# Performance work log

Measured on AMD Instinct MI355X. Metric: run time of the kernel, lower is better.

The kernel has to match this reference:

```python
import jax, jax.numpy as jnp
import numpy as np

B, S, HID = 2, 2048, 2048
H, KV, D, E = 16, 4, 128, 32
NB = 9  # num_behavior + 1
EPS = 1e-6
SCALING = (E + D) ** -0.5


def rmsnorm(x, w, eps=EPS):
    # normalize over last dim in fp32, like Qwen3MoeRMSNorm
    xf = x.astype(jnp.float32)
    var = jnp.mean(xf * xf, axis=-1, keepdims=True)
    return (xf * jax.lax.rsqrt(var + eps)).astype(x.dtype) * w


def setup_inputs() -> dict:
    key = jax.random.key(0)
    ks = jax.random.split(key, 12)
    s = lambda n: 1.0 / np.sqrt(n)
    return {
        "hidden_states": jax.random.normal(ks[0], (B, S, HID), jnp.float32),
        "behavior_index": jax.random.randint(ks[1], (B, S), 0, NB),
        "q_proj_w": jax.random.normal(ks[2], (H * D, HID), jnp.float32) * s(HID),
        "k_proj_w": jax.random.normal(ks[3], (KV * D, HID), jnp.float32) * s(HID),
        "v_proj_w": jax.random.normal(ks[4], (KV * D, HID), jnp.float32) * s(HID),
        "o_proj_w": jax.random.normal(ks[5], (HID, H * D), jnp.float32) * s(H * D),
        "q_norm_w": jnp.ones((D,), jnp.float32),
        "k_norm_w": jnp.ones((D,), jnp.float32),
        "qbe_table": jax.random.normal(ks[6], (NB, H * E), jnp.float32),
        "kbe_table": jax.random.normal(ks[7], (NB, KV * E), jnp.float32),
        "qbn_w": jnp.ones((E,), jnp.float32),
        "kbn_w": jnp.ones((E,), jnp.float32),
    }


def reference(hidden_states, behavior_index, q_proj_w, k_proj_w, v_proj_w,
              o_proj_w, q_norm_w, k_norm_w, qbe_table, kbe_table, qbn_w, kbn_w):
    b, s, _ = hidden_states.shape
    # QKV projections + per-head RMSNorm on q/k
    q = rmsnorm((hidden_states @ q_proj_w.T).reshape(b, s, H, D), q_norm_w)
    k = rmsnorm((hidden_states @ k_proj_w.T).reshape(b, s, KV, D), k_norm_w)
    v = (hidden_states @ v_proj_w.T).reshape(b, s, KV, D)
    q = q.transpose(0, 2, 1, 3)  # [b,H,s,D]
    k = k.transpose(0, 2, 1, 3)  # [b,KV,s,D]
    v = v.transpose(0, 2, 1, 3)  # [b,KV,s,D]
    # behavior embeddings: lookup -> per-head RMSNorm -> concat onto head_dim
    qbe = rmsnorm(qbe_table[behavior_index].reshape(b, s, H, E), qbn_w).transpose(0, 2, 1, 3)
    kbe = rmsnorm(kbe_table[behavior_index].reshape(b, s, KV, E), kbn_w).transpose(0, 2, 1, 3)
    q = jnp.concatenate([q, qbe], axis=-1)  # [b,H,s,D+E]
    k = jnp.concatenate([k, kbe], axis=-1)  # [b,KV,s,D+E]
    # GQA: repeat kv heads
    g = H // KV
    k = jnp.repeat(k, g, axis=1)
    v = jnp.repeat(v, g, axis=1)
    # eager attention, causal, softmax in fp32
    scores = jnp.einsum('bhqd,bhkd->bhqk', q, k) * SCALING
    causal = jnp.tril(jnp.ones((s, s), bool))
    scores = jnp.where(causal, scores, jnp.finfo(scores.dtype).min)
    attn = jax.nn.softmax(scores.astype(jnp.float32), axis=-1).astype(q.dtype)
    out = jnp.einsum('bhqk,bhkd->bhqd', attn, v)  # [b,H,s,D]
    out = out.transpose(0, 2, 1, 3).reshape(b, s, H * D)
    return out @ o_proj_w.T
```

## Files before the change

### kernel.cpp

```cpp
#include <hip/hip_runtime.h>

typedef unsigned short u16;
typedef unsigned int u32;
typedef __bf16 bf16x8 __attribute__((ext_vector_type(8)));
typedef __bf16 b16x4 __attribute__((ext_vector_type(4)));
typedef short s16x4 __attribute__((ext_vector_type(4)));
typedef float f32x4 __attribute__((ext_vector_type(4)));

#define SCALE 0.07905694150420949f
#define LOG2E 1.4426950408889634f

__device__ __forceinline__ float bf2f(u16 h) { return __uint_as_float(((u32)h) << 16); }
__device__ __forceinline__ u16 f2bf(float f) {
  u32 u = __float_as_uint(f);
  u += 0x7fffu + ((u >> 16) & 1u);
  return (u16)(u >> 16);
}
__device__ __forceinline__ u16 f2bf_fast(float f) {
  return (u16)((__float_as_uint(f) + 0x8000u) >> 16);
}
__device__ __forceinline__ bf16x8 ldfrag(const u16* p) {
  int4 t = *reinterpret_cast<const int4*>(p);
  return __builtin_bit_cast(bf16x8, t);
}

__device__ __forceinline__ f32x4 mfma16x16(s16x4 a, s16x4 b, f32x4 c) {
#if __has_builtin(__builtin_amdgcn_mfma_f32_16x16x16bf16_1k)
  return __builtin_amdgcn_mfma_f32_16x16x16bf16_1k(a, b, c, 0, 0, 0);
#elif __has_builtin(__builtin_amdgcn_mfma_f32_16x16x16_bf16)
  return __builtin_amdgcn_mfma_f32_16x16x16_bf16(__builtin_bit_cast(b16x4, a),
                                                 __builtin_bit_cast(b16x4, b), c, 0, 0, 0);
#else
  asm volatile("s_nop 2\n\tv_mfma_f32_16x16x16_bf16 %0, %1, %2, %0"
               : "+v"(c) : "v"(a), "v"(b));
  return c;
#endif
}

__device__ __forceinline__ void gld16(const u16* g, u16* l) {
  __builtin_amdgcn_global_load_lds((const __attribute__((address_space(1))) u32*)(const void*)g,
                                   (__attribute__((address_space(3))) u32*)(void*)l, 16, 0, 0);
}

__global__ void conv_f32_bf16(const float* __restrict__ in, u16* __restrict__ out, int n) {
  int n4 = n >> 2;
  for (int i = blockIdx.x * blockDim.x + threadIdx.x; i < n4; i += gridDim.x * blockDim.x) {
    float4 v = reinterpret_cast<const float4*>(in)[i];
    ushort4 o = {f2bf(v.x), f2bf(v.y), f2bf(v.z), f2bf(v.w)};
    reinterpret_cast<ushort4*>(out)[i] = o;
  }
}

template <int OUT_BF16>
__global__ __launch_bounds__(256, 2) void gemm_bt(const u16* __restrict__ A,
                                                  const u16* __restrict__ Bw,
                                                  void* __restrict__ Cv,
                                                  int M, int N, int K) {
  __shared__ __align__(16) u16 As[2][8192];
  __shared__ __align__(16) u16 Bs[2][8192];
  const int tid = threadIdx.x;
  const int nbn = N >> 7;
  const int cpx = gridDim.x >> 3;
  const int swz = (blockIdx.x & 7) * cpx + (blockIdx.x >> 3);
  const int bm = swz / nbn, bn = swz % nbn;
  const int row0 = bm << 7, col0 = bn << 7;
  const int lane = tid & 63, w = tid >> 6;
  const int lg = lane >> 4, lr = lane & 15;
  const int wr = w >> 1, wc = w & 1;
  const int nt = K >> 6;

  auto stage = [&](int slot, int t) {
    const size_t k0 = (size_t)t << 6;
#pragma unroll
    for (int it = 0; it < 4; ++it) {
      int G = it * 256 + tid;
      int r = G >> 3, p = G & 7;
      int gs = p ^ (r & 7);
      gld16(&A[(size_t)(row0 + r) * K + k0 + gs * 8], &As[slot][(size_t)G * 8]);
      gld16(&Bw[(size_t)(col0 + r) * K + k0 + gs * 8], &Bs[slot][(size_t)G * 8]);
    }
  };

  f32x4 acc[4][4] = {};
  stage(0, 0);
  if (nt > 1) stage(1, 1);

  for (int t = 0; t < nt; ++t) {
    const int slot = t & 1;
    if (t + 1 < nt) {
      asm volatile("s_waitcnt vmcnt(8)" ::: "memory");
    } else {
      asm volatile("s_waitcnt vmcnt(0)" ::: "memory");
    }
    __builtin_amdgcn_s_barrier();
    __builtin_amdgcn_sched_barrier(0);
#pragma unroll
    for (int kk = 0; kk < 2; ++kk) {
      bf16x8 af[4], bv[4];
#pragma unroll
      for (int m = 0; m < 4; ++m) {
        int r = wr * 64 + m * 16 + lr;
        int g = (kk * 4 + lg) ^ (lr & 7);
        af[m] = ldfrag(&As[slot][r * 64 + g * 8]);
      }
#pragma unroll
      for (int n = 0; n < 4; ++n) {
        int r = wc * 64 + n * 16 + lr;
        int g = (kk * 4 + lg) ^ (lr & 7);
        bv[n] = ldfrag(&Bs[slot][r * 64 + g * 8]);
      }
#pragma unroll
      for (int m = 0; m < 4; ++m)
#pragma unroll
        for (int n = 0; n < 4; ++n)
          acc[m][n] = __builtin_amdgcn_mfma_f32_16x16x32_bf16(af[m], bv[n], acc[m][n], 0, 0, 0);
    }
    __builtin_amdgcn_sched_barrier(0);
    __builtin_amdgcn_s_barrier();
    if (t + 2 < nt) stage(slot, t + 2);
  }

#pragma unroll
  for (int m = 0; m < 4; ++m)
#pragma unroll
    for (int n = 0; n < 4; ++n)
#pragma unroll
      for (int r = 0; r < 4; ++r) {
        int row = row0 + wr * 64 + m * 16 + lg * 4 + r;
        int col = col0 + wc * 64 + n * 16 + lr;
        float v = acc[m][n][r];
        if (OUT_BF16)
          ((u16*)Cv)[(size_t)row * N + col] = f2bf(v);
        else
          ((float*)Cv)[(size_t)row * N + col] = v;
      }
}

__global__ __launch_bounds__(256) void postproc(
    const u16* __restrict__ qkv, const int* __restrict__ bidx,
    const float* __restrict__ qnw, const float* __restrict__ knw,
    const float* __restrict__ qbe_t, const float* __restrict__ kbe_t,
    const float* __restrict__ qbn, const float* __restrict__ kbn,
    u16* __restrict__ qcat, u16* __restrict__ kcat, u16* __restrict__ vt) {
  const int tok = blockIdx.x;
  const int b = tok >> 11, s = tok & 2047;
  const int w = threadIdx.x >> 6, lane = threadIdx.x & 63;
  const int idx = bidx[tok];
  const u16* base = qkv + (size_t)tok * 3072;
  const float QS = SCALE * LOG2E;

  for (int h = w; h < 16; h += 4) {
    float x0 = bf2f(base[h * 128 + 2 * lane]);
    float x1 = bf2f(base[h * 128 + 2 * lane + 1]);
    float ss = x0 * x0 + x1 * x1;
#pragma unroll
    for (int o = 32; o; o >>= 1) ss += __shfl_xor(ss, o);
    float rn = rsqrtf(ss * (1.f / 128.f) + 1e-6f) * QS;
    size_t ob = ((size_t)(b * 16 + h) * 2048 + s) * 160;
    qcat[ob + 2 * lane] = f2bf(x0 * rn * qnw[2 * lane]);
    qcat[ob + 2 * lane + 1] = f2bf(x1 * rn * qnw[2 * lane + 1]);
    if (lane < 32) {
      float e = qbe_t[idx * 512 + h * 32 + lane];
      float s2 = e * e;
#pragma unroll
      for (int o = 16; o; o >>= 1) s2 += __shfl_xor(s2, o);
      qcat[ob + 128 + lane] = f2bf(e * rsqrtf(s2 * (1.f / 32.f) + 1e-6f) * qbn[lane] * QS);
    }
  }
  {
    const int kv = w;
    float x0 = bf2f(base[2048 + kv * 128 + 2 * lane]);
    float x1 = bf2f(base[2048 + kv * 128 + 2 * lane + 1]);
    float ss = x0 * x0 + x1 * x1;
#pragma unroll
    for (int o = 32; o; o >>= 1) ss += __shfl_xor(ss, o);
    float rn = rsqrtf(ss * (1.f / 128.f) + 1e-6f);
    size_t ob = ((size_t)(b * 4 + kv) * 2048 + s) * 160;
    kcat[ob + 2 * lane] = f2bf(x0 * rn * knw[2 * lane]);
    kcat[ob + 2 * lane + 1] = f2bf(x1 * rn * knw[2 * lane + 1]);
    if (lane < 32) {
      float e = kbe_t[idx * 128 + kv * 32 + lane];
      float s2 = e * e;
#pragma unroll
      for (int o = 16; o; o >>= 1) s2 += __shfl_xor(s2, o);
      kcat[ob + 128 + lane] = f2bf(e * rsqrtf(s2 * (1.f / 32.f) + 1e-6f) * kbn[lane]);
    }
    size_t vb = (size_t)(b * 4 + kv) * 128 * 2048;
    vt[vb + (size_t)lane * 2048 + s] = base[2560 + kv * 128 + lane];
    vt[vb + (size_t)(lane + 64) * 2048 + s] = base[2560 + kv * 128 + 64 + lane];
  }
}

__global__ __launch_bounds__(256, 2) void attn(const u16* __restrict__ qcat,
                                               const u16* __restrict__ kcat,
                                               const u16* __restrict__ vt,
                                               u16* __restrict__ aout) {
  __shared__ __align__(16) u16 Kls[2][10240];
  __shared__ __align__(16) u16 Vls[8192];
  const int tid = threadIdx.x;
  const int blk = blockIdx.x;
  const int kvh = blk & 3;
  const int b = (blk >> 2) & 1;
  const int hq = (blk >> 3) & 3;
  const int g = blk >> 5;
  const int h = kvh * 4 + hq;
  const int w = tid >> 6;
  const int lane = tid & 63;
  const int lg = lane >> 4, lr = lane & 15;
  const int qb_a = g * 4 + w;
  const int qb_b = 127 - qb_a;
  const int qpa = qb_a * 16 + lr;
  const int qpb = qb_b * 16 + lr;
  const int nt = 32 - g;

  const u16* qpA = qcat + ((size_t)(b * 16 + h) * 2048 + qb_a * 16) * 160;
  const u16* qpB = qcat + ((size_t)(b * 16 + h) * 2048 + qb_b * 16) * 160;
  bf16x8 qfa[5], qfb[5];
#pragma unroll
  for (int c = 0; c < 5; ++c) {
    qfa[c] = ldfrag(qpA + lr * 160 + c * 32 + lg * 8);
    qfb[c] = ldfrag(qpB + lr * 160 + c * 32 + lg * 8);
  }

  const u16* kbp = kcat + (size_t)(b * 4 + kvh) * 2048 * 160;
  const u16* vbp = vt + (size_t)(b * 4 + kvh) * 128 * 2048;

  auto stageK = [&](int buf, int kt) {
    const u16* ksrc = kbp + (size_t)kt * (64 * 160);
#pragma unroll
    for (int it = 0; it < 5; ++it) {
      int G = it * 256 + tid;
      int r = G / 20, p = G - r * 20;
      int gs = p ^ ((r >> 1) & 3);
      gld16(ksrc + r * 160 + gs * 8, &Kls[buf][G * 8]);
    }
  };
  auto stageV = [&](int kt) {
    const u16* vsrc = vbp + kt * 64;
#pragma unroll
    for (int it = 0; it < 4; ++it) {
      int G = it * 256 + tid;
      int r = G >> 3, p = G & 7;
      int gs = p ^ (r & 7);
      gld16(vsrc + (size_t)r * 2048 + gs * 8, &Vls[G * 8]);
    }
  };

  float ma = -INFINITY, la = 0.f, mb = -INFINITY, lb = 0.f;
  f32x4 acc_a[8] = {}, acc_b[8] = {};

  stageK(0, 0);
  stageV(0);
  __syncthreads();

  for (int kt = 0; kt < nt; ++kt) {
    const int buf = kt & 1;
    const bool aact = (kt <= g);
    if (kt + 1 < nt) stageK(buf ^ 1, kt + 1);

    f32x4 sa[4] = {}, sb[4] = {};
#pragma unroll
    for (int c = 0; c < 5; ++c) {
      bf16x8 kf[4];
#pragma unroll
      for (int i = 0; i < 4; ++i) {
        int r = i * 16 + lr;
        int p = (c * 4 + lg) ^ ((r >> 1) & 3);
        kf[i] = ldfrag(&Kls[buf][(r * 20 + p) * 8]);
      }
#pragma unroll
      for (int i = 0; i < 4; ++i)
        sb[i] = __builtin_amdgcn_mfma_f32_16x16x32_bf16(kf[i], qfb[c], sb[i], 0, 0, 0);
      if (aact)
#pragma unroll
        for (int i = 0; i < 4; ++i)
          sa[i] = __builtin_amdgcn_mfma_f32_16x16x32_bf16(kf[i], qfa[c], sa[i], 0, 0, 0);
    }

    s16x4 pka[4], pkb[4];
    auto soft = [&](f32x4 (&st)[4], float& mm, float& ls, f32x4 (&ac)[8], s16x4 (&pk)[4],
                    bool masked, int qpos) {
      float vmax = -INFINITY;
#pragma unroll
      for (int i = 0; i < 4; ++i)
#pragma unroll
        for (int r = 0; r < 4; ++r) {
          float v = st[i][r];
          if (masked && (kt * 64 + i * 16 + 4 * lg + r > qpos)) v = -INFINITY;
          st[i][r] = v;
          vmax = fmaxf(vmax, v);
        }
      vmax = fmaxf(vmax, __shfl_xor(vmax, 16));
      vmax = fmaxf(vmax, __shfl_xor(vmax, 32));
      bool skip = __all(vmax <= mm + 8.f);
      float mn = skip ? mm : fmaxf(mm, vmax);
      float rs = 0.f;
#pragma unroll
      for (int i = 0; i < 4; ++i)
#pragma unroll
        for (int r = 0; r < 4; ++r) {
          float p = exp2f(st[i][r] - mn);
          st[i][r] = p;
          rs += p;
        }
      rs += __shfl_xor(rs, 16);
      rs += __shfl_xor(rs, 32);
      if (skip) {
        ls += rs;
      } else {
        float corr = exp2f(mm - mn);
        ls = ls * corr + rs;
        mm = mn;
        float c4[4];
#pragma unroll
        for (int r = 0; r < 4; ++r) c4[r] = __shfl(corr, 4 * lg + r);
#pragma unroll
        for (int dt = 0; dt < 8; ++dt)
#pragma unroll
          for (int r = 0; r < 4; ++r) ac[dt][r] *= c4[r];
      }
#pragma unroll
      for (int i = 0; i < 4; ++i) {
        pk[i][0] = (short)f2bf_fast(st[i][0]);
        pk[i][1] = (short)f2bf_fast(st[i][1]);
        pk[i][2] = (short)f2bf_fast(st[i][2]);
        pk[i][3] = (short)f2bf_fast(st[i][3]);
      }
    };
    soft(sb, mb, lb, acc_b, pkb, kt == nt - 1, qpb);
    if (aact) soft(sa, ma, la, acc_a, pka, kt == g, qpa);

    __syncthreads();

#pragma unroll
    for (int ks = 0; ks < 4; ++ks) {
      s16x4 vf[8];
#pragma unroll
      for (int dt = 0; dt < 8; ++dt) {
        int r = dt * 16 + lr;
        int p = (ks * 2 + (lg >> 1)) ^ (r & 7);
        vf[dt] = *reinterpret_cast<const s16x4*>(&Vls[(r * 8 + p) * 8 + (lg & 1) * 4]);
      }
#pragma unroll
      for (int dt = 0; dt < 8; ++dt) acc_b[dt] = mfma16x16(pkb[ks], vf[dt], acc_b[dt]);
      if (aact)
#pragma unroll
        for (int dt = 0; dt < 8; ++dt) acc_a[dt] = mfma16x16(pka[ks], vf[dt], acc_a[dt]);
    }

    __syncthreads();
    if (kt + 1 < nt) stageV(kt + 1);
  }

  float inva[4], invb[4];
#pragma unroll
  for (int r = 0; r < 4; ++r) {
    inva[r] = 1.f / __shfl(la, 4 * lg + r);
    invb[r] = 1.f / __shfl(lb, 4 * lg + r);
  }
#pragma unroll
  for (int dt = 0; dt < 8; ++dt)
#pragma unroll
    for (int r = 0; r < 4; ++r) {
      int rowa = qb_a * 16 + 4 * lg + r;
      int rowb = qb_b * 16 + 4 * lg + r;
      aout[((size_t)(b * 2048 + rowa) * 16 + h) * 128 + dt * 16 + lr] =
          f2bf(acc_a[dt][r] * inva[r]);
      aout[((size_t)(b * 2048 + rowb) * 16 + h) * 128 + dt * 16 + lr] =
          f2bf(acc_b[dt][r] * invb[r]);
    }
}

extern "C" void kernel_launch(void* const* d_in, const int* in_sizes, int n_in,
                              void* d_out, int out_size, void* d_ws, size_t ws_size,
                              hipStream_t stream) {
  const float* hs = (const float*)d_in[0];
  const int* bidx = (const int*)d_in[1];
  const float* qw = (const float*)d_in[2];
  const float* kw = (const float*)d_in[3];
  const float* vw = (const float*)d_in[4];
  const float* ow = (const float*)d_in[5];
  const float* qnw = (const float*)d_in[6];
  const float* knw = (const float*)d_in[7];
  const float* qbe_t = (const float*)d_in[8];
  const float* kbe_t = (const float*)d_in[9];
  const float* qbn = (const float*)d_in[10];
  const float* kbn = (const float*)d_in[11];

  u16* ws = (u16*)d_ws;
  u16* hs_bf = ws;
  u16* wqkv = hs_bf + 8388608;
  u16* ow_bf = wqkv + 6291456;
  u16* qkv = ow_bf + 4194304;
  u16* qcat = qkv + 12582912;
  u16* kcat = qcat + 10485760;
  u16* vt = kcat + 2621440;
  u16* attn_o = vt + 2097152;

  conv_f32_bf16<<<2048, 256, 0, stream>>>(hs, hs_bf, 8388608);
  conv_f32_bf16<<<1024, 256, 0, stream>>>(qw, wqkv, 4194304);
  conv_f32_bf16<<<512, 256, 0, stream>>>(kw, wqkv + 4194304, 1048576);
  conv_f32_bf16<<<512, 256, 0, stream>>>(vw, wqkv + 5242880, 1048576);
  conv_f32_bf16<<<1024, 256, 0, stream>>>(ow, ow_bf, 4194304);

  gemm_bt<1><<<dim3((4096 / 128) * (3072 / 128)), 256, 0, stream>>>(
      hs_bf, wqkv, (void*)qkv, 4096, 3072, 2048);

  postproc<<<4096, 256, 0, stream>>>(qkv, bidx, qnw, knw, qbe_t, kbe_t, qbn, kbn,
                                     qcat, kcat, vt);

  attn<<<512, 256, 0, stream>>>(qcat, kcat, vt, attn_o);

  gemm_bt<0><<<dim3((4096 / 128) * (2048 / 128)), 256, 0, stream>>>(
      attn_o, ow_bf, (void*)d_out, 4096, 2048, 2048);
}
```

Before: 229.3 us.

## Enlarge GEMM tiles to 256x256 with 512 threads and fuse conversion kernels

```diff
diff --git a/kernel.cpp b/kernel.cpp
--- a/kernel.cpp
+++ b/kernel.cpp
@@ -42,38 +42,55 @@
                                    (__attribute__((address_space(3))) u32*)(void*)l, 16, 0, 0);
 }
 
-__global__ void conv_f32_bf16(const float* __restrict__ in, u16* __restrict__ out, int n) {
-  int n4 = n >> 2;
-  for (int i = blockIdx.x * blockDim.x + threadIdx.x; i < n4; i += gridDim.x * blockDim.x) {
-    float4 v = reinterpret_cast<const float4*>(in)[i];
+__global__ void conv_all(const float* __restrict__ hs, const float* __restrict__ qw,
+                         const float* __restrict__ kw, const float* __restrict__ vw,
+                         const float* __restrict__ ow, u16* __restrict__ hs_bf,
+                         u16* __restrict__ wqkv, u16* __restrict__ ow_bf) {
+  const int total = 4718592;
+  for (int i = blockIdx.x * blockDim.x + threadIdx.x; i < total; i += gridDim.x * blockDim.x) {
+    const float* src;
+    u16* dst;
+    int j = i;
+    if (j < 2097152) {
+      src = hs; dst = hs_bf;
+    } else if (j < 3145728) {
+      j -= 2097152; src = qw; dst = wqkv;
+    } else if (j < 3407872) {
+      j -= 3145728; src = kw; dst = wqkv + 4194304;
+    } else if (j < 3670016) {
+      j -= 3407872; src = vw; dst = wqkv + 5242880;
+    } else {
+      j -= 3670016; src = ow; dst = ow_bf;
+    }
+    float4 v = reinterpret_cast<const float4*>(src)[j];
     ushort4 o = {f2bf(v.x), f2bf(v.y), f2bf(v.z), f2bf(v.w)};
-    reinterpret_cast<ushort4*>(out)[i] = o;
+    reinterpret_cast<ushort4*>(dst)[j] = o;
   }
 }
 
 template <int OUT_BF16>
-__global__ __launch_bounds__(256, 2) void gemm_bt(const u16* __restrict__ A,
+__global__ __launch_bounds__(512, 2) void gemm_bt(const u16* __restrict__ A,
                                                   const u16* __restrict__ Bw,
                                                   void* __restrict__ Cv,
                                                   int M, int N, int K) {
-  __shared__ __align__(16) u16 As[2][8192];
-  __shared__ __align__(16) u16 Bs[2][8192];
+  __shared__ __align__(16) u16 As[2][16384];
+  __shared__ __align__(16) u16 Bs[2][16384];
   const int tid = threadIdx.x;
-  const int nbn = N >> 7;
+  const int nbn = N >> 8;
   const int cpx = gridDim.x >> 3;
   const int swz = (blockIdx.x & 7) * cpx + (blockIdx.x >> 3);
   const int bm = swz / nbn, bn = swz % nbn;
-  const int row0 = bm << 7, col0 = bn << 7;
+  const int row0 = bm << 8, col0 = bn << 8;
   const int lane = tid & 63, w = tid >> 6;
   const int lg = lane >> 4, lr = lane & 15;
-  const int wr = w >> 1, wc = w & 1;
+  const int wr = w >> 2, wc = w & 3;
   const int nt = K >> 6;
 
   auto stage = [&](int slot, int t) {
     const size_t k0 = (size_t)t << 6;
 #pragma unroll
     for (int it = 0; it < 4; ++it) {
-      int G = it * 256 + tid;
+      int G = it * 512 + tid;
       int r = G >> 3, p = G & 7;
       int gs = p ^ (r & 7);
       gld16(&A[(size_t)(row0 + r) * K + k0 + gs * 8], &As[slot][(size_t)G * 8]);
@@ -81,7 +98,7 @@
     }
   };
 
-  f32x4 acc[4][4] = {};
+  f32x4 acc[8][4] = {};
   stage(0, 0);
   if (nt > 1) stage(1, 1);
 
@@ -96,10 +113,10 @@
     __builtin_amdgcn_sched_barrier(0);
 #pragma unroll
     for (int kk = 0; kk < 2; ++kk) {
-      bf16x8 af[4], bv[4];
-#pragma unroll
-      for (int m = 0; m < 4; ++m) {
-        int r = wr * 64 + m * 16 + lr;
+      bf16x8 af[8], bv[4];
+#pragma unroll
+      for (int m = 0; m < 8; ++m) {
+        int r = wr * 128 + m * 16 + lr;
         int g = (kk * 4 + lg) ^ (lr & 7);
         af[m] = ldfrag(&As[slot][r * 64 + g * 8]);
       }
@@ -110,7 +127,7 @@
         bv[n] = ldfrag(&Bs[slot][r * 64 + g * 8]);
       }
 #pragma unroll
-      for (int m = 0; m < 4; ++m)
+      for (int m = 0; m < 8; ++m)
 #pragma unroll
         for (int n = 0; n < 4; ++n)
           acc[m][n] = __builtin_amdgcn_mfma_f32_16x16x32_bf16(af[m], bv[n], acc[m][n], 0, 0, 0);
@@ -121,12 +138,12 @@
   }
 
 #pragma unroll
-  for (int m = 0; m < 4; ++m)
+  for (int m = 0; m < 8; ++m)
 #pragma unroll
     for (int n = 0; n < 4; ++n)
 #pragma unroll
       for (int r = 0; r < 4; ++r) {
-        int row = row0 + wr * 64 + m * 16 + lg * 4 + r;
+        int row = row0 + wr * 128 + m * 16 + lg * 4 + r;
         int col = col0 + wc * 64 + n * 16 + lr;
         float v = acc[m][n][r];
         if (OUT_BF16)
@@ -397,13 +414,9 @@
   u16* vt = kcat + 2621440;
   u16* attn_o = vt + 2097152;
 
-  conv_f32_bf16<<<2048, 256, 0, stream>>>(hs, hs_bf, 8388608);
-  conv_f32_bf16<<<1024, 256, 0, stream>>>(qw, wqkv, 4194304);
-  conv_f32_bf16<<<512, 256, 0, stream>>>(kw, wqkv + 4194304, 1048576);
-  conv_f32_bf16<<<512, 256, 0, stream>>>(vw, wqkv + 5242880, 1048576);
-  conv_f32_bf16<<<1024, 256, 0, stream>>>(ow, ow_bf, 4194304);
-
-  gemm_bt<1><<<dim3((4096 / 128) * (3072 / 128)), 256, 0, stream>>>(
+  conv_all<<<4608, 256, 0, stream>>>(hs, qw, kw, vw, ow, hs_bf, wqkv, ow_bf);
+
+  gemm_bt<1><<<dim3((4096 / 256) * (3072 / 256)), 512, 0, stream>>>(
       hs_bf, wqkv, (void*)qkv, 4096, 3072, 2048);
 
   postproc<<<4096, 256, 0, stream>>>(qkv, bidx, qnw, knw, qbe_t, kbe_t, qbn, kbn,
@@ -411,6 +424,6 @@
 
   attn<<<512, 256, 0, stream>>>(qcat, kcat, vt, attn_o);
 
-  gemm_bt<0><<<dim3((4096 / 128) * (2048 / 128)), 256, 0, stream>>>(
+  gemm_bt<0><<<dim3((4096 / 256) * (2048 / 256)), 512, 0, stream>>>(
       attn_o, ow_bf, (void*)d_out, 4096, 2048, 2048);
 }
```

New measurement: 250.1 us. 9.0% more time.
